# Kernel optimization log

Hardware: AMD Instinct MI355X
Metric: run time of the kernel (lower is better)

The kernel has to match this reference:

```python
import jax, jax.numpy as jnp
import numpy as np

N_NODES = 50000
N_EDGES = 800000
IN_FEATS = 128
NUM_HEADS = 4
OUT_FEATS = 32
SE_HIDDEN = 1  # num_heads // reduction(4) = 1
NEG_SLOPE = 0.2


def setup_inputs() -> dict:
    key = jax.random.key(0)
    ks = jax.random.split(key, 10)
    feat = jax.random.normal(ks[0], (N_NODES, IN_FEATS), dtype=jnp.float32)
    src = jax.random.randint(ks[1], (N_EDGES,), 0, N_NODES)
    dst = jax.random.randint(ks[2], (N_EDGES,), 0, N_NODES)
    HF = NUM_HEADS * OUT_FEATS
    # learned params (xavier-ish scaling)
    W_fc = jax.random.normal(ks[3], (IN_FEATS, HF), dtype=jnp.float32) * (2.0 / (IN_FEATS + HF)) ** 0.5
    attn_l = jax.random.normal(ks[4], (NUM_HEADS, OUT_FEATS), dtype=jnp.float32) * 0.1
    attn_r = jax.random.normal(ks[5], (NUM_HEADS, OUT_FEATS), dtype=jnp.float32) * 0.1
    se_w1 = jax.random.normal(ks[6], (NUM_HEADS, SE_HIDDEN), dtype=jnp.float32) * 0.5
    se_w2 = jax.random.normal(ks[7], (SE_HIDDEN, NUM_HEADS), dtype=jnp.float32) * 0.5
    W_idn = jax.random.normal(ks[8], (IN_FEATS, HF), dtype=jnp.float32) * (2.0 / (IN_FEATS + HF)) ** 0.5
    return {"feat": feat, "W_fc": W_fc, "attn_l": attn_l, "attn_r": attn_r,
            "se_w1": se_w1, "se_w2": se_w2, "W_idn": W_idn, "src": src, "dst": dst}


def reference(feat, W_fc, attn_l, attn_r, se_w1, se_w2, W_idn, src, dst):
    N = feat.shape[0]
    H, F = attn_l.shape
    # node projection: [N, H, F]
    h = (feat @ W_fc).reshape(N, H, F)
    # per-node attention halves: [N, H]
    el = jnp.einsum('nhf,hf->nh', h, attn_l)
    er = jnp.einsum('nhf,hf->nh', h, attn_r)
    # edge logits (gather) + LeakyReLU: [E, H]
    e = jax.nn.leaky_relu(el[src] + er[dst], NEG_SLOPE)
    # edge-softmax over destination neighborhoods (numerically stable)
    emax = jax.ops.segment_max(e, dst, num_segments=N)
    ex = jnp.exp(e - emax[dst])
    denom = jax.ops.segment_sum(ex, dst, num_segments=N)
    a = ex / denom[dst]  # [E, H]
    # message = attention-weighted source features; scatter-sum to dst: [N, H, F]
    rst = jax.ops.segment_sum(h[src] * a[:, :, None], dst, num_segments=N)
    # SE block over heads: squeeze over F, excite per head
    y = rst.mean(axis=-1)  # [N, H]
    y = jax.nn.sigmoid(jax.nn.relu(y @ se_w1) @ se_w2)  # [N, H]
    rst = rst * y[:, :, None]
    # identity combinator: residual projection of input features
    rst = rst + (feat @ W_idn).reshape(N, H, F)
    return rst
```

## Files before the change

### kernel.cpp

```cpp
#include <hip/hip_runtime.h>
#include <hip/hip_bf16.h>

#define N_NODES 50000
#define N_EDGES 800000
#define IN_FEATS 128
#define NUM_HEADS 4
#define OUT_FEATS 32
#define HF 128
#define NEG_SLOPE 0.2f
#define NB 196
#define CHUNK 4096

typedef __attribute__((ext_vector_type(8))) short bf16x8;
typedef __attribute__((ext_vector_type(4))) float f32x4;

__device__ __forceinline__ unsigned short f2bf(float f) {
    unsigned u = __float_as_uint(f);
    unsigned r = u + 0x7FFFu + ((u >> 16) & 1u);
    return (unsigned short)(r >> 16);
}
__device__ __forceinline__ float bf2f(unsigned short v) {
    return __uint_as_float((unsigned)v << 16);
}

__global__ __launch_bounds__(256) void pack_hist(
    const float* __restrict__ Wfc,
    const float* __restrict__ Widn,
    unsigned short* __restrict__ Bp,
    const int* __restrict__ dst,
    int* __restrict__ bhist)
{
    if (blockIdx.x < 16) {
        const int nt = blockIdx.x;
        const int ks = threadIdx.x >> 6;
        const int l  = threadIdx.x & 63;
        const int col = nt * 16 + (l & 15);
        const int k0  = ks * 32 + (l >> 4) * 8;
        unsigned short v[8];
        #pragma unroll
        for (int j = 0; j < 8; ++j) {
            const int k = k0 + j;
            const float x = (col < HF) ? Wfc[k * HF + col] : Widn[k * HF + (col - HF)];
            v[j] = f2bf(x);
        }
        *(uint4*)&Bp[(size_t)(((nt * 4 + ks) * 64) + l) * 8] = *(const uint4*)v;
    } else {
        __shared__ int lh[NB];
        for (int i = threadIdx.x; i < NB; i += 256) lh[i] = 0;
        __syncthreads();
        const int e0 = (blockIdx.x - 16) * CHUNK;
        for (int k = threadIdx.x; k < CHUNK; k += 256) {
            const int e = e0 + k;
            if (e < N_EDGES) atomicAdd(&lh[dst[e] >> 8], 1);
        }
        __syncthreads();
        for (int i = threadIdx.x; i < NB; i += 256)
            if (lh[i]) atomicAdd(&bhist[i], lh[i]);
    }
}

__global__ __launch_bounds__(256) void gemm_mfma(
    const float* __restrict__ feat,
    const unsigned short* __restrict__ Bp,
    const float* __restrict__ attn_l,
    const float* __restrict__ attn_r,
    unsigned short* __restrict__ h_bf,
    unsigned short* __restrict__ idn_bf,
    float* __restrict__ el,
    float* __restrict__ er)
{
    __shared__ __align__(16) unsigned short As[64 * IN_FEATS];
    const int tid  = threadIdx.x;
    const int row0 = blockIdx.x * 64;

    #pragma unroll
    for (int it = 0; it < 4; ++it) {
        const int chunk = it * 256 + tid;
        const int r  = chunk >> 4;
        const int c8 = (chunk & 15) * 8;
        float4 a = make_float4(0.f, 0.f, 0.f, 0.f);
        float4 b = make_float4(0.f, 0.f, 0.f, 0.f);
        if (row0 + r < N_NODES) {
            a = *(const float4*)&feat[(size_t)(row0 + r) * IN_FEATS + c8];
            b = *(const float4*)&feat[(size_t)(row0 + r) * IN_FEATS + c8 + 4];
        }
        uint4 p;
        p.x = (unsigned)f2bf(a.x) | ((unsigned)f2bf(a.y) << 16);
        p.y = (unsigned)f2bf(a.z) | ((unsigned)f2bf(a.w) << 16);
        p.z = (unsigned)f2bf(b.x) | ((unsigned)f2bf(b.y) << 16);
        p.w = (unsigned)f2bf(b.z) | ((unsigned)f2bf(b.w) << 16);
        const int byte = r * 256 + ((c8 * 2) ^ ((r & 7) << 4));
        *(uint4*)((char*)As + byte) = p;
    }
    __syncthreads();

    const int l    = tid & 63;
    const int w    = tid >> 6;
    const int colq = l & 15;
    const int kg   = l >> 4;

    f32x4 acc[4][4];
    #pragma unroll
    for (int m = 0; m < 4; ++m)
        #pragma unroll
        for (int n = 0; n < 4; ++n)
            acc[m][n] = (f32x4){0.f, 0.f, 0.f, 0.f};

    #pragma unroll
    for (int ks = 0; ks < 4; ++ks) {
        bf16x8 af[4], bfr[4];
        #pragma unroll
        for (int m = 0; m < 4; ++m) {
            const int row  = m * 16 + colq;
            const int byte = row * 256 + ((ks * 64 + kg * 16) ^ ((row & 7) << 4));
            af[m] = *(const bf16x8*)((const char*)As + byte);
        }
        #pragma unroll
        for (int n = 0; n < 4; ++n) {
            const int ng = w * 4 + n;
            bfr[n] = *(const bf16x8*)&Bp[(size_t)(((ng * 4 + ks) * 64) + l) * 8];
        }
        #pragma unroll
        for (int m = 0; m < 4; ++m)
            #pragma unroll
            for (int n = 0; n < 4; ++n)
                acc[m][n] = __builtin_amdgcn_mfma_f32_16x16x32_bf16(
                    af[m], bfr[n], acc[m][n], 0, 0, 0);
    }

    #pragma unroll
    for (int m = 0; m < 4; ++m) {
        #pragma unroll
        for (int n = 0; n < 4; ++n) {
            const int col = w * 64 + n * 16 + colq;
            #pragma unroll
            for (int r = 0; r < 4; ++r) {
                const int row = row0 + m * 16 + kg * 4 + r;
                if (row < N_NODES) {
                    const unsigned short hv = f2bf(acc[m][n][r]);
                    if (col < HF) h_bf[(size_t)row * HF + col] = hv;
                    else          idn_bf[(size_t)row * HF + (col - HF)] = hv;
                }
            }
        }
    }

    if (w < 2) {
        float al_n[4], ar_n[4];
        #pragma unroll
        for (int n = 0; n < 4; ++n) {
            al_n[n] = attn_l[w * 64 + n * 16 + colq];
            ar_n[n] = attn_r[w * 64 + n * 16 + colq];
        }
        #pragma unroll
        for (int m = 0; m < 4; ++m) {
            #pragma unroll
            for (int r = 0; r < 4; ++r) {
                float pl01 = acc[m][0][r] * al_n[0] + acc[m][1][r] * al_n[1];
                float pl23 = acc[m][2][r] * al_n[2] + acc[m][3][r] * al_n[3];
                float pr01 = acc[m][0][r] * ar_n[0] + acc[m][1][r] * ar_n[1];
                float pr23 = acc[m][2][r] * ar_n[2] + acc[m][3][r] * ar_n[3];
                #pragma unroll
                for (int off = 1; off < 16; off <<= 1) {
                    pl01 += __shfl_xor(pl01, off);
                    pl23 += __shfl_xor(pl23, off);
                    pr01 += __shfl_xor(pr01, off);
                    pr23 += __shfl_xor(pr23, off);
                }
                const int row = row0 + m * 16 + kg * 4 + r;
                if (colq == 0 && row < N_NODES) {
                    el[row * 4 + w * 2 + 0] = pl01;
                    el[row * 4 + w * 2 + 1] = pl23;
                    er[row * 4 + w * 2 + 0] = pr01;
                    er[row * 4 + w * 2 + 1] = pr23;
                }
            }
        }
    }
}

__global__ __launch_bounds__(256) void binit_kernel(
    const int* __restrict__ bhist,
    int* __restrict__ bcur,
    int* __restrict__ bstart,
    int* __restrict__ row_start)
{
    __shared__ int lsc[256];
    const int tid = threadIdx.x;
    const int v = (tid < NB) ? bhist[tid] : 0;
    lsc[tid] = v;
    __syncthreads();
    for (int off = 1; off < 256; off <<= 1) {
        const int t = (tid >= off) ? lsc[tid - off] : 0;
        __syncthreads();
        lsc[tid] += t;
        __syncthreads();
    }
    const int excl = lsc[tid] - v;
    if (tid < NB) { bcur[tid] = excl; bstart[tid] = excl; }
    if (tid == 0) row_start[N_NODES] = N_EDGES;
}

__global__ __launch_bounds__(256) void bin_kernel(
    const int* __restrict__ src,
    const int* __restrict__ dst,
    int* __restrict__ bcur,
    unsigned* __restrict__ ebuf)
{
    __shared__ int lh[NB], lcnt[NB], gbase[NB];
    const int tid = threadIdx.x;
    const int e0  = blockIdx.x * CHUNK;
    for (int i = tid; i < NB; i += 256) lh[i] = 0;
    __syncthreads();
    for (int k = tid; k < CHUNK; k += 256) {
        const int e = e0 + k;
        if (e < N_EDGES) atomicAdd(&lh[dst[e] >> 8], 1);
    }
    __syncthreads();
    for (int i = tid; i < NB; i += 256) {
        lcnt[i]  = 0;
        gbase[i] = (lh[i] > 0) ? atomicAdd(&bcur[i], lh[i]) : 0;
    }
    __syncthreads();
    for (int k = tid; k < CHUNK; k += 256) {
        const int e = e0 + k;
        if (e < N_EDGES) {
            const int d = dst[e];
            const int b = d >> 8;
            const int r = atomicAdd(&lcnt[b], 1);
            ebuf[gbase[b] + r] = ((unsigned)d << 16) | (unsigned)src[e];
        }
    }
}

__global__ __launch_bounds__(256) void csr_kernel(
    const unsigned* __restrict__ ebuf,
    const int* __restrict__ bstart,
    int* __restrict__ row_start,
    unsigned short* __restrict__ ssrc)
{
    __shared__ int lh[256], lsc[256], lrk[256];
    const int b   = blockIdx.x;
    const int tid = threadIdx.x;
    const int n0  = b << 8;
    const int R0  = bstart[b];
    const int R1  = (b + 1 < NB) ? bstart[b + 1] : N_EDGES;
    lh[tid] = 0; lrk[tid] = 0;
    __syncthreads();
    for (int i = R0 + tid; i < R1; i += 256)
        atomicAdd(&lh[(ebuf[i] >> 16) & 255], 1);
    __syncthreads();
    const int v = lh[tid];
    lsc[tid] = v;
    __syncthreads();
    for (int off = 1; off < 256; off <<= 1) {
        const int t = (tid >= off) ? lsc[tid - off] : 0;
        __syncthreads();
        lsc[tid] += t;
        __syncthreads();
    }
    const int excl = lsc[tid] - v;
    lh[tid] = excl;
    if (n0 + tid < N_NODES) row_start[n0 + tid] = R0 + excl;
    __syncthreads();
    for (int i = R0 + tid; i < R1; i += 256) {
        const unsigned p  = ebuf[i];
        const int dl = (p >> 16) & 255;
        const int r  = atomicAdd(&lrk[dl], 1);
        ssrc[R0 + lh[dl] + r] = (unsigned short)(p & 0xFFFFu);
    }
}

__global__ __launch_bounds__(256) void msg_kernel(
    const unsigned short* __restrict__ h_bf,
    const unsigned short* __restrict__ idn_bf,
    const float* __restrict__ el,
    const float* __restrict__ er,
    const int* __restrict__ row_start,
    const unsigned short* __restrict__ ssrc,
    const float* __restrict__ se_w1,
    const float* __restrict__ se_w2,
    float* __restrict__ out)
{
    const int wid  = (blockIdx.x * 256 + threadIdx.x) >> 6;
    const int lane = threadIdx.x & 63;
    if (wid >= N_NODES) return;
    const int n   = wid;
    const int q   = lane >> 4;
    const int sub = lane & 15;
    const int hh  = sub >> 2;
    const int f0  = sub * 8;

    const float erh = er[n * 4 + hh];
    const int s0 = row_start[n], s1 = row_start[n + 1];

    float a0 = 0.f, a1 = 0.f, a2 = 0.f, a3 = 0.f;
    float a4 = 0.f, a5 = 0.f, a6 = 0.f, a7 = 0.f;
    float dsum = 0.f;

    for (int i = s0; i < s1; i += 4) {
        const int e   = i + q;
        const bool ok = e < s1;
        const int s   = ssrc[ok ? e : s0];
        float ev = el[s * 4 + hh] + erh;
        ev = ev > 0.f ? ev : NEG_SLOPE * ev;
        ev = fminf(ev, 25.f);
        const float ex = ok ? __expf(ev) : 0.f;
        dsum += ex;
        const uint4 hv = *(const uint4*)&h_bf[(size_t)s * HF + f0];
        a0 = fmaf(ex, bf2f((unsigned short)(hv.x & 0xFFFFu)), a0);
        a1 = fmaf(ex, bf2f((unsigned short)(hv.x >> 16)),     a1);
        a2 = fmaf(ex, bf2f((unsigned short)(hv.y & 0xFFFFu)), a2);
        a3 = fmaf(ex, bf2f((unsigned short)(hv.y >> 16)),     a3);
        a4 = fmaf(ex, bf2f((unsigned short)(hv.z & 0xFFFFu)), a4);
        a5 = fmaf(ex, bf2f((unsigned short)(hv.z >> 16)),     a5);
        a6 = fmaf(ex, bf2f((unsigned short)(hv.w & 0xFFFFu)), a6);
        a7 = fmaf(ex, bf2f((unsigned short)(hv.w >> 16)),     a7);
    }

    dsum += __shfl_xor(dsum, 32); dsum += __shfl_xor(dsum, 16);
    a0 += __shfl_xor(a0, 32); a0 += __shfl_xor(a0, 16);
    a1 += __shfl_xor(a1, 32); a1 += __shfl_xor(a1, 16);
    a2 += __shfl_xor(a2, 32); a2 += __shfl_xor(a2, 16);
    a3 += __shfl_xor(a3, 32); a3 += __shfl_xor(a3, 16);
    a4 += __shfl_xor(a4, 32); a4 += __shfl_xor(a4, 16);
    a5 += __shfl_xor(a5, 32); a5 += __shfl_xor(a5, 16);
    a6 += __shfl_xor(a6, 32); a6 += __shfl_xor(a6, 16);
    a7 += __shfl_xor(a7, 32); a7 += __shfl_xor(a7, 16);

    float m0 = 0.f, m1 = 0.f, m2 = 0.f, m3 = 0.f;
    float m4 = 0.f, m5 = 0.f, m6 = 0.f, m7 = 0.f;
    if (s1 > s0) {
        const float inv = 1.f / dsum;
        m0 = a0 * inv; m1 = a1 * inv; m2 = a2 * inv; m3 = a3 * inv;
        m4 = a4 * inv; m5 = a5 * inv; m6 = a6 * inv; m7 = a7 * inv;
    }

    float part = m0 + m1 + m2 + m3 + m4 + m5 + m6 + m7;
    part += __shfl_xor(part, 1);
    part += __shfl_xor(part, 2);
    const float y  = part * (1.f / 32.f);
    const float y0 = __shfl(y, 0),  y1 = __shfl(y, 4);
    const float y2 = __shfl(y, 8),  y3 = __shfl(y, 12);
    float z = y0 * se_w1[0] + y1 * se_w1[1] + y2 * se_w1[2] + y3 * se_w1[3];
    z = fmaxf(z, 0.f);
    const float gate = 1.f / (1.f + __expf(-z * se_w2[hh]));

    if (q == 0) {
        const uint4 iv = *(const uint4*)&idn_bf[(size_t)n * HF + f0];
        float4 o0, o1;
        o0.x = m0 * gate + bf2f((unsigned short)(iv.x & 0xFFFFu));
        o0.y = m1 * gate + bf2f((unsigned short)(iv.x >> 16));
        o0.z = m2 * gate + bf2f((unsigned short)(iv.y & 0xFFFFu));
        o0.w = m3 * gate + bf2f((unsigned short)(iv.y >> 16));
        o1.x = m4 * gate + bf2f((unsigned short)(iv.z & 0xFFFFu));
        o1.y = m5 * gate + bf2f((unsigned short)(iv.z >> 16));
        o1.z = m6 * gate + bf2f((unsigned short)(iv.w & 0xFFFFu));
        o1.w = m7 * gate + bf2f((unsigned short)(iv.w >> 16));
        *(float4*)&out[(size_t)n * HF + f0]     = o0;
        *(float4*)&out[(size_t)n * HF + f0 + 4] = o1;
    }
}

extern "C" void kernel_launch(void* const* d_in, const int* in_sizes, int n_in,
                              void* d_out, int out_size, void* d_ws, size_t ws_size,
                              hipStream_t stream)
{
    const float* feat   = (const float*)d_in[0];
    const float* Wfc    = (const float*)d_in[1];
    const float* attn_l = (const float*)d_in[2];
    const float* attn_r = (const float*)d_in[3];
    const float* se_w1  = (const float*)d_in[4];
    const float* se_w2  = (const float*)d_in[5];
    const float* Widn   = (const float*)d_in[6];
    const int*   src    = (const int*)d_in[7];
    const int*   dst    = (const int*)d_in[8];
    float* out = (float*)d_out;

    char* ws = (char*)d_ws;
    size_t off = 0;
    auto alloc = [&](size_t bytes) -> void* {
        void* p = ws + off;
        off = (off + bytes + 255) & ~(size_t)255;
        return p;
    };
    unsigned short* h_bf   = (unsigned short*)alloc((size_t)N_NODES * HF * 2);
    unsigned short* idn_bf = (unsigned short*)alloc((size_t)N_NODES * HF * 2);
    unsigned short* Bp     = (unsigned short*)alloc((size_t)IN_FEATS * 256 * 2);
    float* el         = (float*)alloc((size_t)N_NODES * 4 * 4);
    float* er         = (float*)alloc((size_t)N_NODES * 4 * 4);
    int*   bhist      = (int*)alloc((size_t)NB * 4);
    int*   bcur       = (int*)alloc((size_t)NB * 4);
    int*   bstart     = (int*)alloc((size_t)NB * 4);
    int*   row_start  = (int*)alloc((size_t)(N_NODES + 1) * 4);
    unsigned* ebuf    = (unsigned*)alloc((size_t)N_EDGES * 4);
    unsigned short* ssrc = (unsigned short*)alloc((size_t)N_EDGES * 2);

    hipMemsetAsync(bhist, 0, (size_t)NB * 4, stream);

    const int nbin = (N_EDGES + CHUNK - 1) / CHUNK;
    pack_hist<<<16 + nbin, 256, 0, stream>>>(Wfc, Widn, Bp, dst, bhist);
    gemm_mfma<<<(N_NODES + 63) / 64, 256, 0, stream>>>(feat, Bp, attn_l, attn_r,
                                                       h_bf, idn_bf, el, er);
    binit_kernel<<<1, 256, 0, stream>>>(bhist, bcur, bstart, row_start);
    bin_kernel<<<nbin, 256, 0, stream>>>(src, dst, bcur, ebuf);
    csr_kernel<<<NB, 256, 0, stream>>>(ebuf, bstart, row_start, ssrc);
    msg_kernel<<<(N_NODES * 64) / 256, 256, 0, stream>>>(h_bf, idn_bf, el, er, row_start,
                                                         ssrc, se_w1, se_w2, out);
}
```

Baseline: 194.8 us.

## Fuse CSR build into one cooperative kernel and widen message gather per lane

Merges weight packing, histogram, bucket scan, binning and per-bucket CSR sort into a single cooperative kernel that uses grid-wide syncs instead of four separate launches. This removes launch overhead and the inter-kernel drain between the small CSR stages. The message kernel is also remapped so each lane accumulates 16 features and a wave handles 8 edges per iteration, raising memory-level parallelism. The cost is higher register pressure, an extra shuffle reduction step, and a dependence on cooperative launch residency.

```diff
diff --git a/kernel.cpp b/kernel.cpp
--- a/kernel.cpp
+++ b/kernel.cpp
@@ -1,5 +1,8 @@
 #include <hip/hip_runtime.h>
 #include <hip/hip_bf16.h>
+#include <hip/hip_cooperative_groups.h>
+
+namespace cg = cooperative_groups;
 
 #define N_NODES 50000
 #define N_EDGES 800000
@@ -22,18 +25,35 @@
 __device__ __forceinline__ float bf2f(unsigned short v) {
     return __uint_as_float((unsigned)v << 16);
 }
-
-__global__ __launch_bounds__(256) void pack_hist(
+__device__ __forceinline__ void bf2x2(unsigned u, float& lo, float& hi) {
+    lo = __uint_as_float(u << 16);
+    hi = __uint_as_float(u & 0xFFFF0000u);
+}
+
+__global__ __launch_bounds__(256) void build_csr(
     const float* __restrict__ Wfc,
     const float* __restrict__ Widn,
     unsigned short* __restrict__ Bp,
+    const int* __restrict__ src,
     const int* __restrict__ dst,
-    int* __restrict__ bhist)
+    int* __restrict__ bhist,
+    int* __restrict__ bcur,
+    int* __restrict__ bstart,
+    int* __restrict__ row_start,
+    unsigned* __restrict__ ebuf,
+    unsigned short* __restrict__ ssrc)
 {
-    if (blockIdx.x < 16) {
-        const int nt = blockIdx.x;
-        const int ks = threadIdx.x >> 6;
-        const int l  = threadIdx.x & 63;
+    cg::grid_group grid = cg::this_grid();
+    __shared__ int lh[256];
+    __shared__ int aux[256];
+    __shared__ int aux2[256];
+    const int b   = blockIdx.x;
+    const int tid = threadIdx.x;
+
+    if (b < 16) {
+        const int nt = b;
+        const int ks = tid >> 6;
+        const int l  = tid & 63;
         const int col = nt * 16 + (l & 15);
         const int k0  = ks * 32 + (l >> 4) * 8;
         unsigned short v[8];
@@ -44,18 +64,81 @@
             v[j] = f2bf(x);
         }
         *(uint4*)&Bp[(size_t)(((nt * 4 + ks) * 64) + l) * 8] = *(const uint4*)v;
-    } else {
-        __shared__ int lh[NB];
-        for (int i = threadIdx.x; i < NB; i += 256) lh[i] = 0;
+    }
+
+    for (int i = tid; i < NB; i += 256) lh[i] = 0;
+    __syncthreads();
+    const int e0 = b * CHUNK;
+    for (int k = tid; k < CHUNK; k += 256) {
+        const int e = e0 + k;
+        if (e < N_EDGES) atomicAdd(&lh[dst[e] >> 8], 1);
+    }
+    __syncthreads();
+    for (int i = tid; i < NB; i += 256)
+        if (lh[i]) atomicAdd(&bhist[i], lh[i]);
+
+    grid.sync();
+
+    if (b == 0) {
+        const int v = (tid < NB) ? bhist[tid] : 0;
+        aux[tid] = v;
         __syncthreads();
-        const int e0 = (blockIdx.x - 16) * CHUNK;
-        for (int k = threadIdx.x; k < CHUNK; k += 256) {
-            const int e = e0 + k;
-            if (e < N_EDGES) atomicAdd(&lh[dst[e] >> 8], 1);
-        }
+        for (int off = 1; off < 256; off <<= 1) {
+            const int t = (tid >= off) ? aux[tid - off] : 0;
+            __syncthreads();
+            aux[tid] += t;
+            __syncthreads();
+        }
+        const int excl = aux[tid] - v;
+        if (tid < NB) { bcur[tid] = excl; bstart[tid] = excl; }
+        if (tid == 0) row_start[N_NODES] = N_EDGES;
+    }
+
+    grid.sync();
+
+    for (int i = tid; i < NB; i += 256) {
+        aux[i]  = 0;
+        aux2[i] = (lh[i] > 0) ? atomicAdd(&bcur[i], lh[i]) : 0;
+    }
+    __syncthreads();
+    for (int k = tid; k < CHUNK; k += 256) {
+        const int e = e0 + k;
+        if (e < N_EDGES) {
+            const int d  = dst[e];
+            const int bb = d >> 8;
+            const int r  = atomicAdd(&aux[bb], 1);
+            ebuf[aux2[bb] + r] = ((unsigned)d << 16) | (unsigned)src[e];
+        }
+    }
+
+    grid.sync();
+
+    const int n0 = b << 8;
+    const int R0 = bstart[b];
+    const int R1 = (b + 1 < NB) ? bstart[b + 1] : N_EDGES;
+    lh[tid] = 0; aux2[tid] = 0;
+    __syncthreads();
+    for (int i = R0 + tid; i < R1; i += 256)
+        atomicAdd(&lh[(ebuf[i] >> 16) & 255], 1);
+    __syncthreads();
+    const int v4 = lh[tid];
+    aux[tid] = v4;
+    __syncthreads();
+    for (int off = 1; off < 256; off <<= 1) {
+        const int t = (tid >= off) ? aux[tid - off] : 0;
         __syncthreads();
-        for (int i = threadIdx.x; i < NB; i += 256)
-            if (lh[i]) atomicAdd(&bhist[i], lh[i]);
+        aux[tid] += t;
+        __syncthreads();
+    }
+    const int excl4 = aux[tid] - v4;
+    lh[tid] = excl4;
+    if (n0 + tid < N_NODES) row_start[n0 + tid] = R0 + excl4;
+    __syncthreads();
+    for (int i = R0 + tid; i < R1; i += 256) {
+        const unsigned p = ebuf[i];
+        const int dl = (p >> 16) & 255;
+        const int r  = atomicAdd(&aux2[dl], 1);
+        ssrc[R0 + lh[dl] + r] = (unsigned short)(p & 0xFFFFu);
     }
 }
 
@@ -179,98 +262,6 @@
     }
 }
 
-__global__ __launch_bounds__(256) void binit_kernel(
-    const int* __restrict__ bhist,
-    int* __restrict__ bcur,
-    int* __restrict__ bstart,
-    int* __restrict__ row_start)
-{
-    __shared__ int lsc[256];
-    const int tid = threadIdx.x;
-    const int v = (tid < NB) ? bhist[tid] : 0;
-    lsc[tid] = v;
-    __syncthreads();
-    for (int off = 1; off < 256; off <<= 1) {
-        const int t = (tid >= off) ? lsc[tid - off] : 0;
-        __syncthreads();
-        lsc[tid] += t;
-        __syncthreads();
-    }
-    const int excl = lsc[tid] - v;
-    if (tid < NB) { bcur[tid] = excl; bstart[tid] = excl; }
-    if (tid == 0) row_start[N_NODES] = N_EDGES;
-}
-
-__global__ __launch_bounds__(256) void bin_kernel(
-    const int* __restrict__ src,
-    const int* __restrict__ dst,
-    int* __restrict__ bcur,
-    unsigned* __restrict__ ebuf)
-{
-    __shared__ int lh[NB], lcnt[NB], gbase[NB];
-    const int tid = threadIdx.x;
-    const int e0  = blockIdx.x * CHUNK;
-    for (int i = tid; i < NB; i += 256) lh[i] = 0;
-    __syncthreads();
-    for (int k = tid; k < CHUNK; k += 256) {
-        const int e = e0 + k;
-        if (e < N_EDGES) atomicAdd(&lh[dst[e] >> 8], 1);
-    }
-    __syncthreads();
-    for (int i = tid; i < NB; i += 256) {
-        lcnt[i]  = 0;
-        gbase[i] = (lh[i] > 0) ? atomicAdd(&bcur[i], lh[i]) : 0;
-    }
-    __syncthreads();
-    for (int k = tid; k < CHUNK; k += 256) {
-        const int e = e0 + k;
-        if (e < N_EDGES) {
-            const int d = dst[e];
-            const int b = d >> 8;
-            const int r = atomicAdd(&lcnt[b], 1);
-            ebuf[gbase[b] + r] = ((unsigned)d << 16) | (unsigned)src[e];
-        }
-    }
-}
-
-__global__ __launch_bounds__(256) void csr_kernel(
-    const unsigned* __restrict__ ebuf,
-    const int* __restrict__ bstart,
-    int* __restrict__ row_start,
-    unsigned short* __restrict__ ssrc)
-{
-    __shared__ int lh[256], lsc[256], lrk[256];
-    const int b   = blockIdx.x;
-    const int tid = threadIdx.x;
-    const int n0  = b << 8;
-    const int R0  = bstart[b];
-    const int R1  = (b + 1 < NB) ? bstart[b + 1] : N_EDGES;
-    lh[tid] = 0; lrk[tid] = 0;
-    __syncthreads();
-    for (int i = R0 + tid; i < R1; i += 256)
-        atomicAdd(&lh[(ebuf[i] >> 16) & 255], 1);
-    __syncthreads();
-    const int v = lh[tid];
-    lsc[tid] = v;
-    __syncthreads();
-    for (int off = 1; off < 256; off <<= 1) {
-        const int t = (tid >= off) ? lsc[tid - off] : 0;
-        __syncthreads();
-        lsc[tid] += t;
-        __syncthreads();
-    }
-    const int excl = lsc[tid] - v;
-    lh[tid] = excl;
-    if (n0 + tid < N_NODES) row_start[n0 + tid] = R0 + excl;
-    __syncthreads();
-    for (int i = R0 + tid; i < R1; i += 256) {
-        const unsigned p  = ebuf[i];
-        const int dl = (p >> 16) & 255;
-        const int r  = atomicAdd(&lrk[dl], 1);
-        ssrc[R0 + lh[dl] + r] = (unsigned short)(p & 0xFFFFu);
-    }
-}
-
 __global__ __launch_bounds__(256) void msg_kernel(
     const unsigned short* __restrict__ h_bf,
     const unsigned short* __restrict__ idn_bf,
@@ -286,19 +277,20 @@
     const int lane = threadIdx.x & 63;
     if (wid >= N_NODES) return;
     const int n   = wid;
-    const int q   = lane >> 4;
-    const int sub = lane & 15;
-    const int hh  = sub >> 2;
-    const int f0  = sub * 8;
+    const int q   = lane >> 3;
+    const int sub = lane & 7;
+    const int hh  = sub >> 1;
+    const int f0  = sub * 16;
 
     const float erh = er[n * 4 + hh];
     const int s0 = row_start[n], s1 = row_start[n + 1];
 
-    float a0 = 0.f, a1 = 0.f, a2 = 0.f, a3 = 0.f;
-    float a4 = 0.f, a5 = 0.f, a6 = 0.f, a7 = 0.f;
+    float a[16];
+    #pragma unroll
+    for (int j = 0; j < 16; ++j) a[j] = 0.f;
     float dsum = 0.f;
 
-    for (int i = s0; i < s1; i += 4) {
+    for (int i = s0; i < s1; i += 8) {
         const int e   = i + q;
         const bool ok = e < s1;
         const int s   = ssrc[ok ? e : s0];
@@ -307,58 +299,61 @@
         ev = fminf(ev, 25.f);
         const float ex = ok ? __expf(ev) : 0.f;
         dsum += ex;
-        const uint4 hv = *(const uint4*)&h_bf[(size_t)s * HF + f0];
-        a0 = fmaf(ex, bf2f((unsigned short)(hv.x & 0xFFFFu)), a0);
-        a1 = fmaf(ex, bf2f((unsigned short)(hv.x >> 16)),     a1);
-        a2 = fmaf(ex, bf2f((unsigned short)(hv.y & 0xFFFFu)), a2);
-        a3 = fmaf(ex, bf2f((unsigned short)(hv.y >> 16)),     a3);
-        a4 = fmaf(ex, bf2f((unsigned short)(hv.z & 0xFFFFu)), a4);
-        a5 = fmaf(ex, bf2f((unsigned short)(hv.z >> 16)),     a5);
-        a6 = fmaf(ex, bf2f((unsigned short)(hv.w & 0xFFFFu)), a6);
-        a7 = fmaf(ex, bf2f((unsigned short)(hv.w >> 16)),     a7);
-    }
-
-    dsum += __shfl_xor(dsum, 32); dsum += __shfl_xor(dsum, 16);
-    a0 += __shfl_xor(a0, 32); a0 += __shfl_xor(a0, 16);
-    a1 += __shfl_xor(a1, 32); a1 += __shfl_xor(a1, 16);
-    a2 += __shfl_xor(a2, 32); a2 += __shfl_xor(a2, 16);
-    a3 += __shfl_xor(a3, 32); a3 += __shfl_xor(a3, 16);
-    a4 += __shfl_xor(a4, 32); a4 += __shfl_xor(a4, 16);
-    a5 += __shfl_xor(a5, 32); a5 += __shfl_xor(a5, 16);
-    a6 += __shfl_xor(a6, 32); a6 += __shfl_xor(a6, 16);
-    a7 += __shfl_xor(a7, 32); a7 += __shfl_xor(a7, 16);
-
-    float m0 = 0.f, m1 = 0.f, m2 = 0.f, m3 = 0.f;
-    float m4 = 0.f, m5 = 0.f, m6 = 0.f, m7 = 0.f;
-    if (s1 > s0) {
-        const float inv = 1.f / dsum;
-        m0 = a0 * inv; m1 = a1 * inv; m2 = a2 * inv; m3 = a3 * inv;
-        m4 = a4 * inv; m5 = a5 * inv; m6 = a6 * inv; m7 = a7 * inv;
-    }
-
-    float part = m0 + m1 + m2 + m3 + m4 + m5 + m6 + m7;
+        const uint4 hv0 = *(const uint4*)&h_bf[(size_t)s * HF + f0];
+        const uint4 hv1 = *(const uint4*)&h_bf[(size_t)s * HF + f0 + 8];
+        float lo, hi;
+        bf2x2(hv0.x, lo, hi); a[0]  = fmaf(ex, lo, a[0]);  a[1]  = fmaf(ex, hi, a[1]);
+        bf2x2(hv0.y, lo, hi); a[2]  = fmaf(ex, lo, a[2]);  a[3]  = fmaf(ex, hi, a[3]);
+        bf2x2(hv0.z, lo, hi); a[4]  = fmaf(ex, lo, a[4]);  a[5]  = fmaf(ex, hi, a[5]);
+        bf2x2(hv0.w, lo, hi); a[6]  = fmaf(ex, lo, a[6]);  a[7]  = fmaf(ex, hi, a[7]);
+        bf2x2(hv1.x, lo, hi); a[8]  = fmaf(ex, lo, a[8]);  a[9]  = fmaf(ex, hi, a[9]);
+        bf2x2(hv1.y, lo, hi); a[10] = fmaf(ex, lo, a[10]); a[11] = fmaf(ex, hi, a[11]);
+        bf2x2(hv1.z, lo, hi); a[12] = fmaf(ex, lo, a[12]); a[13] = fmaf(ex, hi, a[13]);
+        bf2x2(hv1.w, lo, hi); a[14] = fmaf(ex, lo, a[14]); a[15] = fmaf(ex, hi, a[15]);
+    }
+
+    dsum += __shfl_xor(dsum, 32);
+    dsum += __shfl_xor(dsum, 16);
+    dsum += __shfl_xor(dsum, 8);
+    #pragma unroll
+    for (int j = 0; j < 16; ++j) {
+        a[j] += __shfl_xor(a[j], 32);
+        a[j] += __shfl_xor(a[j], 16);
+        a[j] += __shfl_xor(a[j], 8);
+    }
+
+    const float inv = (s1 > s0) ? 1.f / dsum : 0.f;
+    #pragma unroll
+    for (int j = 0; j < 16; ++j) a[j] *= inv;
+
+    float part = 0.f;
+    #pragma unroll
+    for (int j = 0; j < 16; ++j) part += a[j];
     part += __shfl_xor(part, 1);
-    part += __shfl_xor(part, 2);
     const float y  = part * (1.f / 32.f);
-    const float y0 = __shfl(y, 0),  y1 = __shfl(y, 4);
-    const float y2 = __shfl(y, 8),  y3 = __shfl(y, 12);
+    const float y0 = __shfl(y, 0), y1 = __shfl(y, 2);
+    const float y2 = __shfl(y, 4), y3 = __shfl(y, 6);
     float z = y0 * se_w1[0] + y1 * se_w1[1] + y2 * se_w1[2] + y3 * se_w1[3];
     z = fmaxf(z, 0.f);
     const float gate = 1.f / (1.f + __expf(-z * se_w2[hh]));
 
     if (q == 0) {
-        const uint4 iv = *(const uint4*)&idn_bf[(size_t)n * HF + f0];
-        float4 o0, o1;
-        o0.x = m0 * gate + bf2f((unsigned short)(iv.x & 0xFFFFu));
-        o0.y = m1 * gate + bf2f((unsigned short)(iv.x >> 16));
-        o0.z = m2 * gate + bf2f((unsigned short)(iv.y & 0xFFFFu));
-        o0.w = m3 * gate + bf2f((unsigned short)(iv.y >> 16));
-        o1.x = m4 * gate + bf2f((unsigned short)(iv.z & 0xFFFFu));
-        o1.y = m5 * gate + bf2f((unsigned short)(iv.z >> 16));
-        o1.z = m6 * gate + bf2f((unsigned short)(iv.w & 0xFFFFu));
-        o1.w = m7 * gate + bf2f((unsigned short)(iv.w >> 16));
-        *(float4*)&out[(size_t)n * HF + f0]     = o0;
-        *(float4*)&out[(size_t)n * HF + f0 + 4] = o1;
+        const uint4 iv0 = *(const uint4*)&idn_bf[(size_t)n * HF + f0];
+        const uint4 iv1 = *(const uint4*)&idn_bf[(size_t)n * HF + f0 + 8];
+        float o[16], lo, hi;
+        bf2x2(iv0.x, lo, hi); o[0]  = fmaf(a[0],  gate, lo); o[1]  = fmaf(a[1],  gate, hi);
+        bf2x2(iv0.y, lo, hi); o[2]  = fmaf(a[2],  gate, lo); o[3]  = fmaf(a[3],  gate, hi);
+        bf2x2(iv0.z, lo, hi); o[4]  = fmaf(a[4],  gate, lo); o[5]  = fmaf(a[5],  gate, hi);
+        bf2x2(iv0.w, lo, hi); o[6]  = fmaf(a[6],  gate, lo); o[7]  = fmaf(a[7],  gate, hi);
+        bf2x2(iv1.x, lo, hi); o[8]  = fmaf(a[8],  gate, lo); o[9]  = fmaf(a[9],  gate, hi);
+        bf2x2(iv1.y, lo, hi); o[10] = fmaf(a[10], gate, lo); o[11] = fmaf(a[11], gate, hi);
+        bf2x2(iv1.z, lo, hi); o[12] = fmaf(a[12], gate, lo); o[13] = fmaf(a[13], gate, hi);
+        bf2x2(iv1.w, lo, hi); o[14] = fmaf(a[14], gate, lo); o[15] = fmaf(a[15], gate, hi);
+        float* op = &out[(size_t)n * HF + f0];
+        *(float4*)&op[0]  = make_float4(o[0],  o[1],  o[2],  o[3]);
+        *(float4*)&op[4]  = make_float4(o[4],  o[5],  o[6],  o[7]);
+        *(float4*)&op[8]  = make_float4(o[8],  o[9],  o[10], o[11]);
+        *(float4*)&op[12] = make_float4(o[12], o[13], o[14], o[15]);
     }
 }
 
@@ -398,13 +393,19 @@
 
     hipMemsetAsync(bhist, 0, (size_t)NB * 4, stream);
 
-    const int nbin = (N_EDGES + CHUNK - 1) / CHUNK;
-    pack_hist<<<16 + nbin, 256, 0, stream>>>(Wfc, Widn, Bp, dst, bhist);
+    {
+        const float* a0 = Wfc;  const float* a1 = Widn;
+        unsigned short* a2 = Bp;
+        const int* a3 = src;    const int* a4 = dst;
+        int* a5 = bhist; int* a6 = bcur; int* a7 = bstart; int* a8 = row_start;
+        unsigned* a9 = ebuf; unsigned short* a10 = ssrc;
+        void* args[] = {&a0, &a1, &a2, &a3, &a4, &a5, &a6, &a7, &a8, &a9, &a10};
+        hipLaunchCooperativeKernel((void*)build_csr, dim3(NB), dim3(256),
+                                   args, 0, stream);
+    }
+
     gemm_mfma<<<(N_NODES + 63) / 64, 256, 0, stream>>>(feat, Bp, attn_l, attn_r,
                                                        h_bf, idn_bf, el, er);
-    binit_kernel<<<1, 256, 0, stream>>>(bhist, bcur, bstart, row_start);
-    bin_kernel<<<nbin, 256, 0, stream>>>(src, dst, bcur, ebuf);
-    csr_kernel<<<NB, 256, 0, stream>>>(ebuf, bstart, row_start, ssrc);
     msg_kernel<<<(N_NODES * 64) / 256, 256, 0, stream>>>(h_bf, idn_bf, el, er, row_start,
                                                          ssrc, se_w1, se_w2, out);
 }
```

Result: slower. 269.3 us (+38.2%).
